# Kernel tuning notes

Hardware: AMD Instinct MI355X
Metric: run time of the kernel (lower is better)

The kernel has to match this reference:

```python
import jax, jax.numpy as jnp
import numpy as np
import math

# static config (mirrors Model.__init__)
NUM_SEGMENTS = 4
TILE = 32
NUM_SEQS = 8
Q_LEN = 128           # query tokens per sequence (uniform)
SEQ_LEN = 2048        # total seq len (context + query)
NUM_Q_HEADS = 32
NUM_KV_HEADS = 8
HEAD_SIZE = 128       # == head_size_padded (required for the torch code to type-check)
BLK_SIZE = 16
MAX_BLOCKS = SEQ_LEN // BLK_SIZE
NUM_BLKS = NUM_SEQS * MAX_BLOCKS


def setup_inputs() -> dict:
    key = jax.random.key(0)
    k1, k2, k3, k4 = jax.random.split(key, 4)
    num_tokens = NUM_SEQS * Q_LEN
    query = jax.random.normal(k1, (num_tokens, NUM_Q_HEADS, HEAD_SIZE), jnp.float32)
    # torch indexes key_cache[pb, kv, :, off, 0] -> 5D with trailing singleton
    key_cache = jax.random.normal(k2, (NUM_BLKS, NUM_KV_HEADS, HEAD_SIZE, BLK_SIZE, 1), jnp.float32)
    value_cache = jax.random.normal(k3, (NUM_BLKS, NUM_KV_HEADS, HEAD_SIZE, BLK_SIZE), jnp.float32)
    # scattered (permuted) physical block assignment, vLLM-style
    block_tables = jax.random.permutation(k4, NUM_BLKS).reshape(NUM_SEQS, MAX_BLOCKS).astype(jnp.int32)
    seq_lens = jnp.full((NUM_SEQS,), SEQ_LEN, dtype=jnp.int32)
    query_start_len = jnp.arange(NUM_SEQS + 1, dtype=jnp.int32) * Q_LEN
    return {
        "query": query,
        "key_cache": key_cache,
        "value_cache": value_cache,
        "block_tables": block_tables,
        "seq_lens": seq_lens,
        "query_start_len": query_start_len,
        "scale": 1.0 / math.sqrt(HEAD_SIZE),
        "k_scale": 1.0,
        "v_scale": 1.0,
        "softcap": 30.0,
    }


def _paged_segmented_attention(query, key_cache, value_cache, block_tables, seq_lens, scale, softcap):
    S, M = block_tables.shape
    T, H, D = query.shape
    Hkv = key_cache.shape[1]
    G = H // Hkv                  # queries per kv head (GQA)
    B = key_cache.shape[3]
    Q = T // S                    # uniform query length per sequence
    L = M * B                     # KV length covered by the block table
    # block-table gather of paged KV -> [S, Hkv, L, D]
    k_all = key_cache[block_tables][..., 0]                              # [S, M, Hkv, D, B]
    k_all = jnp.transpose(k_all, (0, 2, 1, 4, 3)).reshape(S, Hkv, L, D)
    v_all = jnp.transpose(value_cache[block_tables], (0, 2, 1, 4, 3)).reshape(S, Hkv, L, D)
    q = query.reshape(S, Q, Hkv, G, D).astype(jnp.float32)
    scores = scale * jnp.einsum('sqhgd,shld->shgql', q, k_all.astype(jnp.float32))  # [S,Hkv,G,Q,L]
    if softcap > 0:
        scores = softcap * jnp.tanh(scores / softcap)
    ctx = seq_lens - Q                                                   # context length per seq [S]
    qabs = ctx[:, None] + jnp.arange(Q)[None, :]                         # absolute q positions [S,Q]
    kpos = jnp.arange(L)
    causal = kpos[None, None, :] <= qabs[:, :, None]                     # [S,Q,L]
    # keys per segment = tiles_per_segment * 32, per sequence
    span = (-(-seq_lens // (NUM_SEGMENTS * TILE))) * TILE                # [S]
    neg_inf = jnp.float32(-jnp.inf)
    v32 = v_all.astype(jnp.float32)
    outs = []
    for seg in range(NUM_SEGMENTS):                                      # small fixed loop
        seg_mask = (kpos[None, :] >= seg * span[:, None]) & (kpos[None, :] < (seg + 1) * span[:, None])  # [S,L]
        mask = (causal & seg_mask[:, None, :])[:, None, None, :, :]      # [S,1,1,Q,L]
        masked = jnp.where(mask, scores, neg_inf)
        m = masked.max(axis=-1)
        m_safe = jnp.where(m > neg_inf, m, 0.0)                          # torch's zero-clamp of -inf max
        p = jnp.exp(masked - m_safe[..., None])                          # [S,Hkv,G,Q,L]
        # NOTE: torch returns the UNNORMALIZED accumulator (expsum is discarded)
        acc = jnp.einsum('shgql,shld->shgqd', p, v32)
        outs.append(acc)
    out = jnp.stack(outs, axis=-2)                                       # [S,Hkv,G,Q,NSEG,D]
    out = jnp.transpose(out, (0, 3, 1, 2, 4, 5)).reshape(T, H, NUM_SEGMENTS, D)
    return out.astype(query.dtype)


def reference(query, key_cache, value_cache, block_tables, seq_lens, query_start_len, scale, k_scale, v_scale, softcap):
    # fp32 cache path: k_scale/v_scale dequantization is a no-op (torch applies it only for fp8 caches).
    # query_start_len is consistent with uniform Q_LEN per sequence (used implicitly via reshape).
    return _paged_segmented_attention(query, key_cache, value_cache, block_tables, seq_lens,
                                      float(scale), float(softcap))
```

## Files before the change

kernel.cpp:

```cpp
#include <hip/hip_runtime.h>

#define NSEQ   8
#define QLEN   128
#define NQH    32
#define NKVH   8
#define GQ     4
#define HD     128
#define BLK    16
#define MAXBLK 128
#define LTOT   2048
#define NSEGC  4
#define TILEC  32

typedef __attribute__((ext_vector_type(8)))  short  shortx8;
typedef __attribute__((ext_vector_type(4)))  short  shortx4;
typedef __attribute__((ext_vector_type(16))) float  floatx16;
typedef __attribute__((ext_vector_type(4)))  float  fx4;

__device__ __forceinline__ short f2bf(float f) {
    unsigned u = __float_as_uint(f);
    u = (u + 0x7FFFu + ((u >> 16) & 1u)) >> 16;
    return (short)(unsigned short)u;
}

__global__ __launch_bounds__(512, 2) void psa_kernel(
    const float* __restrict__ query,
    const float* __restrict__ key_cache,
    const float* __restrict__ value_cache,
    const int*   __restrict__ block_tables,
    const int*   __restrict__ seq_lens,
    const float* __restrict__ scale_p,
    const float* __restrict__ softcap_p,
    float* __restrict__ out)
{
    __shared__ __align__(16) short kbuf[2][16][64][8];
    __shared__ __align__(16) short vbuf[2][8][128][8];
    __shared__ __align__(16) short pbuf[8][8][32][8];

    const int bi   = blockIdx.x;
    const int p_lo = bi & 7;
    const int qh   = (bi >> 3) & 1;
    const int pp   = (bi >> 4) * 8 + p_lo;
    const int seg  = pp & 3;
    const int h    = (pp >> 2) & 7;
    const int s    = pp >> 5;

    const int tid  = threadIdx.x;
    const int w    = tid >> 6;
    const int lane = tid & 63;
    const int lo   = lane & 31;
    const int hi   = lane >> 5;

    const float NEG_INF = -__builtin_inff();
    const float scale   = *scale_p;
    const float softcap = *softcap_p;
    const int   seq     = seq_lens[s];
    const int   ctx     = seq - QLEN;
    const int   span    = ((seq + NSEGC * TILEC - 1) / (NSEGC * TILEC)) * TILEC;
    const int   seg_start = seg * span;
    int seg_len = LTOT - seg_start;
    if (seg_len > span) seg_len = span;
    const int NT = (seg_len > 0) ? ((seg_len + 63) >> 6) : 0;

    const float LOG2E = 1.4426950408889634f;
    const bool  do_cap = (softcap > 0.0f);
    const float c1 = do_cap ? (2.0f * LOG2E / softcap) : 0.0f;
    const float c2 = do_cap ? (softcap * LOG2E) : 0.0f;

    const int r_base = qh * 256 + w * 32;
    const int qb     = r_base & 127;
    const int g      = r_base >> 7;
    const int qrow   = qb + lo;
    const int q_off  = ((s * QLEN + qrow) * NQH + h * GQ + g) * HD;
    shortx8 qfrag[8];
#pragma unroll
    for (int ks = 0; ks < 8; ++ks) {
        const float* qp = query + q_off + ks * 16 + hi * 8;
        fx4 a = *(const fx4*)qp;
        fx4 b = *(const fx4*)(qp + 4);
        shortx8 v8;
        v8[0] = f2bf(a[0] * scale); v8[1] = f2bf(a[1] * scale);
        v8[2] = f2bf(a[2] * scale); v8[3] = f2bf(a[3] * scale);
        v8[4] = f2bf(b[0] * scale); v8[5] = f2bf(b[1] * scale);
        v8[6] = f2bf(b[2] * scale); v8[7] = f2bf(b[3] * scale);
        qfrag[ks] = v8;
    }

    const int bt_base = s * MAXBLK;

    float kreg[2][8];
    fx4   vreg[2][2];
    const int kb  = tid & 63;
    const int kdc = tid >> 6;
    const int vd  = tid & 127;
    const int vlh = tid >> 7;

    auto stage_load = [&](int nt) {
        {
            int l_glob = seg_start + nt * 64 + kb;
            if (l_glob >= LTOT) l_glob = LTOT - 1;
            const int pb = block_tables[bt_base + (l_glob >> 4)];
            const float* kp = key_cache + (pb * NKVH + h) * (HD * BLK) + (l_glob & 15);
#pragma unroll
            for (int ic = 0; ic < 2; ++ic)
#pragma unroll
                for (int j = 0; j < 8; ++j)
                    kreg[ic][j] = kp[((kdc + ic * 8) * 8 + j) * BLK];
        }
        {
#pragma unroll
            for (int ic = 0; ic < 2; ++ic) {
                const int lslab = vlh + ic * 4;
                int l_glob = seg_start + nt * 64 + lslab * 8;
                if (l_glob >= LTOT) l_glob = LTOT - 8;
                const int pb = block_tables[bt_base + (l_glob >> 4)];
                const float* vp = value_cache + ((pb * NKVH + h) * HD + vd) * BLK + (l_glob & 15);
                vreg[ic][0] = *(const fx4*)vp;
                vreg[ic][1] = *(const fx4*)(vp + 4);
            }
        }
    };
    auto stage_write = [&](int bb) {
#pragma unroll
        for (int ic = 0; ic < 2; ++ic) {
            shortx8 v8;
#pragma unroll
            for (int j = 0; j < 8; ++j) v8[j] = f2bf(kreg[ic][j]);
            *(shortx8*)(&kbuf[bb][kdc + ic * 8][kb][0]) = v8;
        }
#pragma unroll
        for (int ic = 0; ic < 2; ++ic) {
            shortx8 v8;
#pragma unroll
            for (int j = 0; j < 4; ++j) {
                v8[j]     = f2bf(vreg[ic][0][j]);
                v8[4 + j] = f2bf(vreg[ic][1][j]);
            }
            *(shortx8*)(&vbuf[bb][vlh + ic * 4][vd][0]) = v8;
        }
    };

    floatx16 acc[4];
#pragma unroll
    for (int dt = 0; dt < 4; ++dt)
#pragma unroll
        for (int i = 0; i < 16; ++i) acc[dt][i] = 0.0f;
    float m_run = NEG_INF;

    if (NT > 0) { stage_load(0); stage_write(0); }

    for (int nt = 0; nt < NT; ++nt) {
        const int bb = nt & 1;
        __syncthreads();
        const bool pre = (nt + 1 < NT);
        if (pre) stage_load(nt + 1);

        const int tile_l0 = seg_start + nt * 64;
        const bool need_mask = (tile_l0 + 63 > ctx + qb) || (nt * 64 + 63 >= seg_len);

#pragma unroll
        for (int nsub = 0; nsub < 2; ++nsub) {
            floatx16 c;
#pragma unroll
            for (int i = 0; i < 16; ++i) c[i] = 0.0f;
#pragma unroll
            for (int ks = 0; ks < 8; ++ks) {
                shortx8 af = *(const shortx8*)(&kbuf[bb][ks * 2 + hi][nsub * 32 + lo][0]);
                c = __builtin_amdgcn_mfma_f32_32x32x16_bf16(af, qfrag[ks], c, 0, 0, 0);
            }
            float z[16];
            float mloc = NEG_INF;
#pragma unroll
            for (int r = 0; r < 16; ++r) {
                const float si = c[r];
                float zz;
                if (do_cap) {
                    const float u  = __builtin_amdgcn_exp2f(si * c1);
                    const float rr = __builtin_amdgcn_rcpf(u + 1.0f);
                    zz = c2 - (2.0f * c2) * rr;
                } else {
                    zz = si * LOG2E;
                }
                if (need_mask) {
                    const int key   = nsub * 32 + (r & 3) + 8 * (r >> 2) + 4 * hi;
                    const int l_loc = nt * 64 + key;
                    const bool ok = (l_loc < seg_len) && (tile_l0 + key <= ctx + qb + lo);
                    zz = ok ? zz : NEG_INF;
                }
                z[r] = zz;
                mloc = fmaxf(mloc, zz);
            }
            mloc  = fmaxf(mloc, __shfl_xor(mloc, 32, 64));
            m_run = fmaxf(m_run, mloc);
#pragma unroll
            for (int rq = 0; rq < 4; ++rq) {
                shortx4 pk;
#pragma unroll
                for (int i = 0; i < 4; ++i)
                    pk[i] = f2bf(__builtin_amdgcn_exp2f(z[rq * 4 + i]));
                *(shortx4*)(&pbuf[w][nsub * 4 + rq][lo][hi * 4]) = pk;
            }
        }

#pragma unroll
        for (int ks = 0; ks < 4; ++ks) {
            shortx8 pf = *(const shortx8*)(&pbuf[w][ks * 2 + hi][lo][0]);
#pragma unroll
            for (int dt = 0; dt < 4; ++dt) {
                shortx8 vf = *(const shortx8*)(&vbuf[bb][ks * 2 + hi][dt * 32 + lo][0]);
                acc[dt] = __builtin_amdgcn_mfma_f32_32x32x16_bf16(pf, vf, acc[dt], 0, 0, 0);
            }
        }

        if (pre) stage_write(bb ^ 1);
    }

    const float scv = (m_run == NEG_INF) ? 0.0f : __builtin_amdgcn_exp2f(-m_run);
    const int out_base = ((s * QLEN + qb) * NQH + (h * GQ + g)) * (NSEGC * HD) + seg * HD + lo;
#pragma unroll
    for (int r = 0; r < 16; ++r) {
        const int row = (r & 3) + 8 * (r >> 2) + 4 * hi;
        const float sc = __shfl(scv, row, 64);
        const int ob = out_base + row * (NQH * NSEGC * HD);
#pragma unroll
        for (int dt = 0; dt < 4; ++dt)
            out[ob + dt * 32] = acc[dt][r] * sc;
    }
}

extern "C" void kernel_launch(void* const* d_in, const int* in_sizes, int n_in,
                              void* d_out, int out_size, void* d_ws, size_t ws_size,
                              hipStream_t stream) {
    const float* query        = (const float*)d_in[0];
    const float* key_cache    = (const float*)d_in[1];
    const float* value_cache  = (const float*)d_in[2];
    const int*   block_tables = (const int*)d_in[3];
    const int*   seq_lens     = (const int*)d_in[4];
    const float* scale_p      = (const float*)d_in[6];
    const float* softcap_p    = (const float*)d_in[9];

    psa_kernel<<<dim3(512), dim3(512), 0, stream>>>(
        query, key_cache, value_cache, block_tables, seq_lens,
        scale_p, softcap_p, (float*)d_out);
}
```

Measured before the change: 236.9 us.

## Shrink KV tile to 32, skip fully masked tiles, pass P via shuffles

The KV tile shrinks from 64 to 32 keys, which cuts shared memory and raises the launch-bounds occupancy target from 2 to 4 blocks. Tiles lying entirely past the causal limit for a wave's query rows now skip both MFMA stages. P is no longer staged through a shared-memory buffer; the bf16 P fragments are rearranged with cross-lane shuffles. The running max is now tracked on raw scores and mapped through softcap only at the end, which relies on softcap being monotonic. In exchange there are twice as many barrier iterations, and the higher occupancy target may cause register spilling.

```diff
diff --git a/kernel.cpp b/kernel.cpp
--- a/kernel.cpp
+++ b/kernel.cpp
@@ -13,17 +13,20 @@
 #define TILEC  32
 
 typedef __attribute__((ext_vector_type(8)))  short  shortx8;
-typedef __attribute__((ext_vector_type(4)))  short  shortx4;
 typedef __attribute__((ext_vector_type(16))) float  floatx16;
 typedef __attribute__((ext_vector_type(4)))  float  fx4;
+typedef __attribute__((ext_vector_type(4)))  unsigned int uintx4;
 
 __device__ __forceinline__ short f2bf(float f) {
     unsigned u = __float_as_uint(f);
     u = (u + 0x7FFFu + ((u >> 16) & 1u)) >> 16;
     return (short)(unsigned short)u;
 }
-
-__global__ __launch_bounds__(512, 2) void psa_kernel(
+__device__ __forceinline__ unsigned pack2bf(float a, float b) {
+    return (unsigned)(unsigned short)f2bf(a) | ((unsigned)(unsigned short)f2bf(b) << 16);
+}
+
+__global__ __launch_bounds__(512, 4) void psa_kernel(
     const float* __restrict__ query,
     const float* __restrict__ key_cache,
     const float* __restrict__ value_cache,
@@ -33,9 +36,8 @@
     const float* __restrict__ softcap_p,
     float* __restrict__ out)
 {
-    __shared__ __align__(16) short kbuf[2][16][64][8];
-    __shared__ __align__(16) short vbuf[2][8][128][8];
-    __shared__ __align__(16) short pbuf[8][8][32][8];
+    __shared__ __align__(16) short kbuf[2][16][32][8];
+    __shared__ __align__(16) short vbuf[2][4][128][8];
 
     const int bi   = blockIdx.x;
     const int p_lo = bi & 7;
@@ -60,7 +62,7 @@
     const int   seg_start = seg * span;
     int seg_len = LTOT - seg_start;
     if (seg_len > span) seg_len = span;
-    const int NT = (seg_len > 0) ? ((seg_len + 63) >> 6) : 0;
+    const int NT = (seg_len > 0) ? ((seg_len + 31) >> 5) : 0;
 
     const float LOG2E = 1.4426950408889634f;
     const bool  do_cap = (softcap > 0.0f);
@@ -87,57 +89,47 @@
     }
 
     const int bt_base = s * MAXBLK;
-
-    float kreg[2][8];
-    fx4   vreg[2][2];
-    const int kb  = tid & 63;
-    const int kdc = tid >> 6;
+    const int ctxq    = ctx + qb;
+    const int ctxql   = ctxq + lo;
+
+    float kreg[8];
+    fx4   vreg[2];
+    const int kb  = tid & 31;
+    const int kdc = tid >> 5;
     const int vd  = tid & 127;
     const int vlh = tid >> 7;
 
     auto stage_load = [&](int nt) {
         {
-            int l_glob = seg_start + nt * 64 + kb;
+            int l_glob = seg_start + nt * 32 + kb;
             if (l_glob >= LTOT) l_glob = LTOT - 1;
             const int pb = block_tables[bt_base + (l_glob >> 4)];
             const float* kp = key_cache + (pb * NKVH + h) * (HD * BLK) + (l_glob & 15);
 #pragma unroll
-            for (int ic = 0; ic < 2; ++ic)
-#pragma unroll
-                for (int j = 0; j < 8; ++j)
-                    kreg[ic][j] = kp[((kdc + ic * 8) * 8 + j) * BLK];
+            for (int j = 0; j < 8; ++j)
+                kreg[j] = kp[(kdc * 8 + j) * BLK];
         }
         {
-#pragma unroll
-            for (int ic = 0; ic < 2; ++ic) {
-                const int lslab = vlh + ic * 4;
-                int l_glob = seg_start + nt * 64 + lslab * 8;
-                if (l_glob >= LTOT) l_glob = LTOT - 8;
-                const int pb = block_tables[bt_base + (l_glob >> 4)];
-                const float* vp = value_cache + ((pb * NKVH + h) * HD + vd) * BLK + (l_glob & 15);
-                vreg[ic][0] = *(const fx4*)vp;
-                vreg[ic][1] = *(const fx4*)(vp + 4);
-            }
+            int l_glob = seg_start + nt * 32 + vlh * 8;
+            if (l_glob >= LTOT) l_glob = LTOT - 8;
+            const int pb = block_tables[bt_base + (l_glob >> 4)];
+            const float* vp = value_cache + ((pb * NKVH + h) * HD + vd) * BLK + (l_glob & 15);
+            vreg[0] = *(const fx4*)vp;
+            vreg[1] = *(const fx4*)(vp + 4);
         }
     };
     auto stage_write = [&](int bb) {
-#pragma unroll
-        for (int ic = 0; ic < 2; ++ic) {
-            shortx8 v8;
-#pragma unroll
-            for (int j = 0; j < 8; ++j) v8[j] = f2bf(kreg[ic][j]);
-            *(shortx8*)(&kbuf[bb][kdc + ic * 8][kb][0]) = v8;
-        }
-#pragma unroll
-        for (int ic = 0; ic < 2; ++ic) {
-            shortx8 v8;
-#pragma unroll
-            for (int j = 0; j < 4; ++j) {
-                v8[j]     = f2bf(vreg[ic][0][j]);
-                v8[4 + j] = f2bf(vreg[ic][1][j]);
-            }
-            *(shortx8*)(&vbuf[bb][vlh + ic * 4][vd][0]) = v8;
-        }
+        shortx8 v8;
+#pragma unroll
+        for (int j = 0; j < 8; ++j) v8[j] = f2bf(kreg[j]);
+        *(shortx8*)(&kbuf[bb][kdc][kb][0]) = v8;
+        shortx8 w8;
+#pragma unroll
+        for (int j = 0; j < 4; ++j) {
+            w8[j]     = f2bf(vreg[0][j]);
+            w8[4 + j] = f2bf(vreg[1][j]);
+        }
+        *(shortx8*)(&vbuf[bb][vlh][vd][0]) = w8;
     };
 
     floatx16 acc[4];
@@ -155,67 +147,90 @@
         const bool pre = (nt + 1 < NT);
         if (pre) stage_load(nt + 1);
 
-        const int tile_l0 = seg_start + nt * 64;
-        const bool need_mask = (tile_l0 + 63 > ctx + qb) || (nt * 64 + 63 >= seg_len);
-
-#pragma unroll
-        for (int nsub = 0; nsub < 2; ++nsub) {
+        const int tile_l0 = seg_start + nt * 32;
+        if (tile_l0 <= ctxq + 31) {
+            const bool need_mask = (tile_l0 + 31 > ctxq) || (nt * 32 + 31 >= seg_len);
+
             floatx16 c;
 #pragma unroll
             for (int i = 0; i < 16; ++i) c[i] = 0.0f;
 #pragma unroll
             for (int ks = 0; ks < 8; ++ks) {
-                shortx8 af = *(const shortx8*)(&kbuf[bb][ks * 2 + hi][nsub * 32 + lo][0]);
+                shortx8 af = *(const shortx8*)(&kbuf[bb][ks * 2 + hi][lo][0]);
                 c = __builtin_amdgcn_mfma_f32_32x32x16_bf16(af, qfrag[ks], c, 0, 0, 0);
             }
-            float z[16];
-            float mloc = NEG_INF;
-#pragma unroll
-            for (int r = 0; r < 16; ++r) {
-                const float si = c[r];
-                float zz;
-                if (do_cap) {
-                    const float u  = __builtin_amdgcn_exp2f(si * c1);
-                    const float rr = __builtin_amdgcn_rcpf(u + 1.0f);
-                    zz = c2 - (2.0f * c2) * rr;
-                } else {
-                    zz = si * LOG2E;
+
+            unsigned pkl[4], pkh[4];
+#pragma unroll
+            for (int q4 = 0; q4 < 4; ++q4) {
+                float p[4];
+#pragma unroll
+                for (int j = 0; j < 4; ++j) {
+                    const float si = c[q4 * 4 + j];
+                    float pv;
+                    if (do_cap) {
+                        const float u  = __builtin_amdgcn_exp2f(si * c1);
+                        const float rr = __builtin_amdgcn_rcpf(u + 1.0f);
+                        pv = __builtin_amdgcn_exp2f(fmaf(-2.0f * c2, rr, c2));
+                    } else {
+                        pv = __builtin_amdgcn_exp2f(si * LOG2E);
+                    }
+                    bool ok = true;
+                    if (need_mask) {
+                        const int key   = j + 8 * q4 + 4 * hi;
+                        const int l_loc = nt * 32 + key;
+                        ok = (l_loc < seg_len) && (tile_l0 + key <= ctxql);
+                        pv = ok ? pv : 0.0f;
+                    }
+                    m_run = ok ? fmaxf(m_run, si) : m_run;
+                    p[j] = pv;
                 }
-                if (need_mask) {
-                    const int key   = nsub * 32 + (r & 3) + 8 * (r >> 2) + 4 * hi;
-                    const int l_loc = nt * 64 + key;
-                    const bool ok = (l_loc < seg_len) && (tile_l0 + key <= ctx + qb + lo);
-                    zz = ok ? zz : NEG_INF;
+                pkl[q4] = pack2bf(p[0], p[1]);
+                pkh[q4] = pack2bf(p[2], p[3]);
+            }
+
+            unsigned otl[4], oth[4];
+#pragma unroll
+            for (int q4 = 0; q4 < 4; ++q4) {
+                otl[q4] = __shfl_xor(pkl[q4], 32, 64);
+                oth[q4] = __shfl_xor(pkh[q4], 32, 64);
+            }
+
+#pragma unroll
+            for (int ksl = 0; ksl < 2; ++ksl) {
+                const int qe = 2 * ksl, qo = 2 * ksl + 1;
+                uintx4 pu;
+                pu[0] = hi ? otl[qo] : pkl[qe];
+                pu[1] = hi ? oth[qo] : pkh[qe];
+                pu[2] = hi ? pkl[qo] : otl[qe];
+                pu[3] = hi ? pkh[qo] : oth[qe];
+                const shortx8 pf = __builtin_bit_cast(shortx8, pu);
+#pragma unroll
+                for (int dt = 0; dt < 4; ++dt) {
+                    shortx8 vf = *(const shortx8*)(&vbuf[bb][ksl * 2 + hi][dt * 32 + lo][0]);
+                    acc[dt] = __builtin_amdgcn_mfma_f32_32x32x16_bf16(pf, vf, acc[dt], 0, 0, 0);
                 }
-                z[r] = zz;
-                mloc = fmaxf(mloc, zz);
-            }
-            mloc  = fmaxf(mloc, __shfl_xor(mloc, 32, 64));
-            m_run = fmaxf(m_run, mloc);
-#pragma unroll
-            for (int rq = 0; rq < 4; ++rq) {
-                shortx4 pk;
-#pragma unroll
-                for (int i = 0; i < 4; ++i)
-                    pk[i] = f2bf(__builtin_amdgcn_exp2f(z[rq * 4 + i]));
-                *(shortx4*)(&pbuf[w][nsub * 4 + rq][lo][hi * 4]) = pk;
-            }
-        }
-
-#pragma unroll
-        for (int ks = 0; ks < 4; ++ks) {
-            shortx8 pf = *(const shortx8*)(&pbuf[w][ks * 2 + hi][lo][0]);
-#pragma unroll
-            for (int dt = 0; dt < 4; ++dt) {
-                shortx8 vf = *(const shortx8*)(&vbuf[bb][ks * 2 + hi][dt * 32 + lo][0]);
-                acc[dt] = __builtin_amdgcn_mfma_f32_32x32x16_bf16(pf, vf, acc[dt], 0, 0, 0);
             }
         }
 
         if (pre) stage_write(bb ^ 1);
     }
 
-    const float scv = (m_run == NEG_INF) ? 0.0f : __builtin_amdgcn_exp2f(-m_run);
+    m_run = fmaxf(m_run, __shfl_xor(m_run, 32, 64));
+    float scv;
+    if (m_run == NEG_INF) {
+        scv = 0.0f;
+    } else {
+        float zmax;
+        if (do_cap) {
+            const float u  = __builtin_amdgcn_exp2f(m_run * c1);
+            const float rr = __builtin_amdgcn_rcpf(u + 1.0f);
+            zmax = fmaf(-2.0f * c2, rr, c2);
+        } else {
+            zmax = m_run * LOG2E;
+        }
+        scv = __builtin_amdgcn_exp2f(-zmax);
+    }
     const int out_base = ((s * QLEN + qb) * NQH + (h * GQ + g)) * (NSEGC * HD) + seg * HD + lo;
 #pragma unroll
     for (int r = 0; r < 16; ++r) {
```

After: 313.7 us. +32.4%, slower.
